# Kernel optimization log

Measured on AMD Instinct MI355X. Metric: run time of the kernel, lower is better.

## Reference

```python
import jax, jax.numpy as jnp
import numpy as np

EMBED_DIM = 2048
NUM_HEADS = 16
LATENT_DIM = 512
HEAD_DIM = EMBED_DIM // NUM_HEADS


def setup_inputs() -> dict:
    key = jax.random.key(0)
    ks = jax.random.split(key, 9)
    s = 0.02
    x = jax.random.normal(ks[0], (2, 2048, EMBED_DIM), dtype=jnp.float32)
    # torch Linear weights stored as [out, in]
    q_w = jax.random.normal(ks[1], (EMBED_DIM, EMBED_DIM), jnp.float32) * s
    q_b = jax.random.normal(ks[2], (EMBED_DIM,), jnp.float32) * s
    kvd_w = jax.random.normal(ks[3], (LATENT_DIM, EMBED_DIM), jnp.float32) * s
    kvd_b = jax.random.normal(ks[4], (LATENT_DIM,), jnp.float32) * s
    kvu_w = jax.random.normal(ks[5], (EMBED_DIM * 2, LATENT_DIM), jnp.float32) * s
    kvu_b = jax.random.normal(ks[6], (EMBED_DIM * 2,), jnp.float32) * s
    out_w = jax.random.normal(ks[7], (EMBED_DIM, EMBED_DIM), jnp.float32) * s
    out_b = jax.random.normal(ks[8], (EMBED_DIM,), jnp.float32) * s
    return {"x": x, "q_w": q_w, "q_b": q_b, "kvd_w": kvd_w, "kvd_b": kvd_b,
            "kvu_w": kvu_w, "kvu_b": kvu_b, "out_w": out_w, "out_b": out_b}


def reference(x, q_w, q_b, kvd_w, kvd_b, kvu_w, kvu_b, out_w, out_b):
    b, s, _ = x.shape
    q = x @ q_w.T + q_b                      # [b,s,E]
    latent = x @ kvd_w.T + kvd_b             # [b,s,L]
    kv = latent @ kvu_w.T + kvu_b            # [b,s,2E]
    k, v = kv[..., :EMBED_DIM], kv[..., EMBED_DIM:]
    def heads(t):
        return t.reshape(b, s, NUM_HEADS, HEAD_DIM).transpose(0, 2, 1, 3)  # [b,h,s,d]
    qh, kh, vh = heads(q), heads(k), heads(v)
    scores = jnp.einsum('bhqd,bhkd->bhqk', qh, kh) / jnp.sqrt(jnp.float32(HEAD_DIM))
    attn = jax.nn.softmax(scores, axis=-1)
    out = jnp.einsum('bhqk,bhkd->bhqd', attn, vh)
    out = out.transpose(0, 2, 1, 3).reshape(b, s, EMBED_DIM)
    return out @ out_w.T + out_b
```

## Files before the change

### kernel.cpp

```cpp
#include <hip/hip_runtime.h>

typedef unsigned short u16;
typedef __attribute__((ext_vector_type(8))) __bf16 bf16x8;
typedef __attribute__((ext_vector_type(8))) unsigned short u16x8;
typedef __attribute__((ext_vector_type(4))) float f32x4;
typedef __attribute__((ext_vector_type(16))) float f32x16;

#define BK 32
#define TILE_ELEMS (128 * BK)
#define QSCALE 0.12753706518066536f

#if __has_builtin(__builtin_amdgcn_exp2f)
#define EXP2(x) __builtin_amdgcn_exp2f(x)
#else
#define EXP2(x) exp2f(x)
#endif

__device__ __forceinline__ u16 f32_to_bf16(float f) {
  __bf16 h = (__bf16)f;
  return __builtin_bit_cast(u16, h);
}

__device__ __forceinline__ void gll16(const u16* g, u16* l) {
  __builtin_amdgcn_global_load_lds(
      (const __attribute__((address_space(1))) void*)g,
      (__attribute__((address_space(3))) void*)l, 16, 0, 0);
}

__global__ __launch_bounds__(256) void cvt_all(
    const float* __restrict__ x, const float* __restrict__ qw,
    const float* __restrict__ kvdw, const float* __restrict__ kvuw,
    const float* __restrict__ outw, u16* __restrict__ X, u16* __restrict__ W1,
    u16* __restrict__ W2, u16* __restrict__ W3, u16* __restrict__ W4) {
  int blk = blockIdx.x;
  const float* src;
  u16* dst;
  int base;
  if (blk < 8192)       { src = x;    dst = X;  base = blk; }
  else if (blk < 12288) { src = qw;   dst = W1; base = blk - 8192; }
  else if (blk < 13312) { src = kvdw; dst = W2; base = blk - 12288; }
  else if (blk < 15360) { src = kvuw; dst = W3; base = blk - 13312; }
  else                  { src = outw; dst = W4; base = blk - 15360; }
  int i = base * 1024 + threadIdx.x * 4;
  float4 v = *(const float4*)(src + i);
  ushort4 o;
  o.x = f32_to_bf16(v.x);
  o.y = f32_to_bf16(v.y);
  o.z = f32_to_bf16(v.z);
  o.w = f32_to_bf16(v.w);
  *(ushort4*)(dst + i) = o;
}

__device__ __forceinline__ void gemm_core(const u16* __restrict__ A_tile,
                                          const u16* __restrict__ B_tile, int K,
                                          u16* As, u16* Bs, f32x4 acc[4][4]) {
  const int tid = threadIdx.x;
  const int w = tid >> 6, lane = tid & 63;
  const int wm = (w >> 1) << 6, wn = (w & 1) << 6;
  const int quad = lane >> 4, l15 = lane & 15;

  const u16* Ap = A_tile + (tid >> 2) * K + (tid & 3) * 8;
  const u16* Bp = B_tile + (tid >> 2) * K + (tid & 3) * 8;
  u16* Asw = As + w * 512;
  u16* Bsw = Bs + w * 512;

  gll16(Ap, Asw);
  gll16(Ap + 64 * K, Asw + 2048);
  gll16(Bp, Bsw);
  gll16(Bp + 64 * K, Bsw + 2048);

  int p = 0;
  for (int k0 = 0; k0 < K; k0 += BK) {
    const int kn = k0 + BK;
    __syncthreads();
    if (kn < K) {
      const int off = (p ^ 1) * TILE_ELEMS;
      gll16(Ap + kn, Asw + off);
      gll16(Ap + 64 * K + kn, Asw + off + 2048);
      gll16(Bp + kn, Bsw + off);
      gll16(Bp + 64 * K + kn, Bsw + off + 2048);
    }
    const u16* Asr = As + p * TILE_ELEMS;
    const u16* Bsr = Bs + p * TILE_ELEMS;
    bf16x8 af[4], bf[4];
#pragma unroll
    for (int i = 0; i < 4; i++)
      af[i] = *(const bf16x8*)(Asr + (wm + i * 16 + l15) * BK + quad * 8);
#pragma unroll
    for (int j = 0; j < 4; j++)
      bf[j] = *(const bf16x8*)(Bsr + (wn + j * 16 + l15) * BK + quad * 8);
#pragma unroll
    for (int i = 0; i < 4; i++)
#pragma unroll
      for (int j = 0; j < 4; j++)
        acc[i][j] =
            __builtin_amdgcn_mfma_f32_16x16x32_bf16(af[i], bf[j], acc[i][j], 0, 0, 0);
    p ^= 1;
  }
}

__global__ __launch_bounds__(256) void gemm_qlat(const u16* __restrict__ X,
                                                 const u16* __restrict__ QW,
                                                 const u16* __restrict__ KVDW,
                                                 const float* __restrict__ q_b,
                                                 const float* __restrict__ kvd_b,
                                                 u16* __restrict__ Qb,
                                                 u16* __restrict__ Lat) {
  __shared__ __align__(16) u16 As[2 * TILE_ELEMS];
  __shared__ __align__(16) u16 Bs[2 * TILE_ELEMS];
  const int bn = blockIdx.x, bm = blockIdx.y;
  const bool isq = bn < 16;
  const u16* B_tile = isq ? QW + (size_t)bn * 128 * 2048
                          : KVDW + (size_t)(bn - 16) * 128 * 2048;
  f32x4 acc[4][4];
  const f32x4 z = {0.f, 0.f, 0.f, 0.f};
#pragma unroll
  for (int i = 0; i < 4; i++)
#pragma unroll
    for (int j = 0; j < 4; j++) acc[i][j] = z;
  gemm_core(X + (size_t)bm * 128 * 2048, B_tile, 2048, As, Bs, acc);

  const float* bias = isq ? q_b : kvd_b;
  u16* C = isq ? Qb : Lat;
  const int N = isq ? 2048 : 512;
  const float scale = isq ? QSCALE : 1.0f;
  const int colbase = (isq ? bn : bn - 16) * 128;

  const int tid = threadIdx.x;
  const int w = tid >> 6, lane = tid & 63;
  const int wm = (w >> 1) << 6, wn = (w & 1) << 6;
  const int quad = lane >> 4, l15 = lane & 15;
  const int row0 = bm * 128 + wm + quad * 4;
  const int col0 = colbase + wn + l15;
#pragma unroll
  for (int i = 0; i < 4; i++)
#pragma unroll
    for (int j = 0; j < 4; j++) {
      int col = col0 + j * 16;
      float bv = bias[col];
#pragma unroll
      for (int r = 0; r < 4; r++) {
        int row = row0 + i * 16 + r;
        C[(size_t)row * N + col] = f32_to_bf16((acc[i][j][r] + bv) * scale);
      }
    }
}

__global__ __launch_bounds__(256) void gemm_f32out(const u16* __restrict__ A,
                                                   const u16* __restrict__ B,
                                                   const float* __restrict__ bias,
                                                   float* __restrict__ C, int K, int N) {
  __shared__ __align__(16) u16 As[2 * TILE_ELEMS];
  __shared__ __align__(16) u16 Bs[2 * TILE_ELEMS];
  f32x4 acc[4][4];
  const f32x4 z = {0.f, 0.f, 0.f, 0.f};
#pragma unroll
  for (int i = 0; i < 4; i++)
#pragma unroll
    for (int j = 0; j < 4; j++) acc[i][j] = z;
  gemm_core(A + (size_t)blockIdx.y * 128 * K, B + (size_t)blockIdx.x * 128 * K, K,
            As, Bs, acc);

  const int tid = threadIdx.x;
  const int w = tid >> 6, lane = tid & 63;
  const int wm = (w >> 1) << 6, wn = (w & 1) << 6;
  const int quad = lane >> 4, l15 = lane & 15;
  const int row0 = blockIdx.y * 128 + wm + quad * 4;
  const int col0 = blockIdx.x * 128 + wn + l15;
#pragma unroll
  for (int i = 0; i < 4; i++)
#pragma unroll
    for (int j = 0; j < 4; j++) {
      int col = col0 + j * 16;
      float bv = bias[col];
#pragma unroll
      for (int r = 0; r < 4; r++) {
        int row = row0 + i * 16 + r;
        C[(size_t)row * N + col] = acc[i][j][r] + bv;
      }
    }
}

__global__ __launch_bounds__(256) void gemm_kv(const u16* __restrict__ A,
                                               const u16* __restrict__ B,
                                               const float* __restrict__ bias,
                                               u16* __restrict__ Khat,
                                               u16* __restrict__ Vt, int K) {
  __shared__ __align__(16) u16 As[2 * TILE_ELEMS];
  __shared__ __align__(16) u16 Bs[2 * TILE_ELEMS];
  f32x4 acc[4][4];
  const f32x4 z = {0.f, 0.f, 0.f, 0.f};
#pragma unroll
  for (int i = 0; i < 4; i++)
#pragma unroll
    for (int j = 0; j < 4; j++) acc[i][j] = z;
  gemm_core(A + (size_t)blockIdx.y * 128 * K, B + (size_t)blockIdx.x * 128 * K, K,
            As, Bs, acc);

  const int tid = threadIdx.x;
  const int w = tid >> 6, lane = tid & 63;
  const int wm = (w >> 1) << 6, wn = (w & 1) << 6;
  const int quad = lane >> 4, l15 = lane & 15;
  const int row0 = blockIdx.y * 128 + wm + quad * 4;
  const int col0 = blockIdx.x * 128 + wn + l15;
#pragma unroll
  for (int i = 0; i < 4; i++)
#pragma unroll
    for (int j = 0; j < 4; j++) {
      int n = col0 + j * 16;
      float bv = bias[n];
#pragma unroll
      for (int r = 0; r < 4; r++) {
        int row = row0 + i * 16 + r;
        int bb = row >> 11, s = row & 2047;
        u16 val = f32_to_bf16(acc[i][j][r] + bv);
        if (n < 2048) {
          int h = n >> 7, d = n & 127;
          Khat[((size_t)(bb * 16 + h) * 2048 + s) * 128 + d] = val;
        } else {
          int h = (n - 2048) >> 7, d = n & 127;
          Vt[((size_t)(bb * 16 + h) * 128 + d) * 2048 + s] = val;
        }
      }
    }
}

__global__ __launch_bounds__(256) void attn_kernel(const u16* __restrict__ Q,
                                                   const u16* __restrict__ Khat,
                                                   const u16* __restrict__ Vt,
                                                   u16* __restrict__ O) {
  __shared__ __align__(16) u16 Ks[2][32 * 136];
  __shared__ __align__(16) u16 Vs[2][128 * 40];

  const int tid = threadIdx.x;
  const int w = tid >> 6, lane = tid & 63;
  const int l31 = lane & 31, half = lane >> 5;
  const int qt = blockIdx.x & 15;
  const int h = (blockIdx.x >> 4) & 15;
  const int b = blockIdx.x >> 8;
  const int bh = b * 16 + h;

  bf16x8 qf[8];
  {
    const u16* qrow = Q + (size_t)(b * 2048 + qt * 128 + w * 32 + l31) * 2048 +
                      h * 128 + half * 8;
#pragma unroll
    for (int kc = 0; kc < 8; kc++) qf[kc] = *(const bf16x8*)(qrow + kc * 16);
  }

  f32x16 oacc[4];
#pragma unroll
  for (int nt = 0; nt < 4; nt++)
#pragma unroll
    for (int r = 0; r < 16; r++) oacc[nt][r] = 0.f;
  float ls0 = 0.f, ls1 = 0.f, ls2 = 0.f, ls3 = 0.f;

  const u16* Kg = Khat + (size_t)bh * 2048 * 128;
  const u16* Vg = Vt + (size_t)bh * 128 * 2048;

  const int kkr = tid >> 4, kc0 = tid & 15;
  const int vd = tid >> 2, vc0 = tid & 3;
  const int vlo = (vc0 >> 1) * 16 + (vc0 & 1) * 4;
  const int vhi = vlo + 8;

  u16x8 kv[2], vv[2];
#pragma unroll
  for (int it = 0; it < 2; it++) {
    kv[it] = *(const u16x8*)(Kg + (size_t)(kkr + it * 16) * 128 + kc0 * 8);
    vv[it] = *(const u16x8*)(Vg + (size_t)(vd + it * 64) * 2048 + vc0 * 8);
  }
#pragma unroll
  for (int it = 0; it < 2; it++) {
    *(u16x8*)(Ks[0] + (kkr + it * 16) * 136 + kc0 * 8) = kv[it];
    const unsigned long long* vp = (const unsigned long long*)&vv[it];
    *(unsigned long long*)(Vs[0] + (vd + it * 64) * 40 + vlo) = vp[0];
    *(unsigned long long*)(Vs[0] + (vd + it * 64) * 40 + vhi) = vp[1];
  }

  int p = 0;
  for (int key0 = 0; key0 < 2048; key0 += 32) {
    const int kn = (key0 + 32 < 2048) ? (key0 + 32) : 0;
#pragma unroll
    for (int it = 0; it < 2; it++) {
      kv[it] = *(const u16x8*)(Kg + (size_t)(kn + kkr + it * 16) * 128 + kc0 * 8);
      vv[it] = *(const u16x8*)(Vg + (size_t)(vd + it * 64) * 2048 + kn + vc0 * 8);
    }
    __syncthreads();

    f32x16 sacc;
#pragma unroll
    for (int r = 0; r < 16; r++) sacc[r] = 0.f;
#pragma unroll
    for (int kc = 0; kc < 8; kc++) {
      bf16x8 kf = *(const bf16x8*)(Ks[p] + l31 * 136 + kc * 16 + half * 8);
      sacc = __builtin_amdgcn_mfma_f32_32x32x16_bf16(kf, qf[kc], sacc, 0, 0, 0);
    }

    float e[16];
#pragma unroll
    for (int r = 0; r < 16; r++) e[r] = EXP2(sacc[r]);
    ls0 += e[0] + e[4] + e[8] + e[12];
    ls1 += e[1] + e[5] + e[9] + e[13];
    ls2 += e[2] + e[6] + e[10] + e[14];
    ls3 += e[3] + e[7] + e[11] + e[15];
    bf16x8 pa0, pa1;
#pragma unroll
    for (int i = 0; i < 8; i++) {
      pa0[i] = (__bf16)e[i];
      pa1[i] = (__bf16)e[8 + i];
    }

#pragma unroll
    for (int nt = 0; nt < 4; nt++) {
      bf16x8 vf0 = *(const bf16x8*)(Vs[p] + (nt * 32 + l31) * 40 + half * 8);
      bf16x8 vf1 = *(const bf16x8*)(Vs[p] + (nt * 32 + l31) * 40 + 16 + half * 8);
      oacc[nt] = __builtin_amdgcn_mfma_f32_32x32x16_bf16(pa0, vf0, oacc[nt], 0, 0, 0);
      oacc[nt] = __builtin_amdgcn_mfma_f32_32x32x16_bf16(pa1, vf1, oacc[nt], 0, 0, 0);
    }

    const int pn = p ^ 1;
#pragma unroll
    for (int it = 0; it < 2; it++) {
      *(u16x8*)(Ks[pn] + (kkr + it * 16) * 136 + kc0 * 8) = kv[it];
      const unsigned long long* vp = (const unsigned long long*)&vv[it];
      *(unsigned long long*)(Vs[pn] + (vd + it * 64) * 40 + vlo) = vp[0];
      *(unsigned long long*)(Vs[pn] + (vd + it * 64) * 40 + vhi) = vp[1];
    }
    p = pn;
  }

  float lsum = (ls0 + ls1) + (ls2 + ls3);
  lsum += __shfl_xor(lsum, 32);
  float inv = 1.0f / lsum;
  float wr[16];
#pragma unroll
  for (int r = 0; r < 16; r++) {
    int ridx = (r & 3) + 8 * (r >> 2) + 4 * half;
    wr[r] = __shfl(inv, ridx);
  }

#pragma unroll
  for (int nt = 0; nt < 4; nt++)
#pragma unroll
    for (int r = 0; r < 16; r++) {
      int ridx = (r & 3) + 8 * (r >> 2) + 4 * half;
      int row = b * 2048 + qt * 128 + w * 32 + ridx;
      int col = h * 128 + nt * 32 + l31;
      O[(size_t)row * 2048 + col] = f32_to_bf16(oacc[nt][r] * wr[r]);
    }
}

extern "C" void kernel_launch(void* const* d_in, const int* in_sizes, int n_in,
                              void* d_out, int out_size, void* d_ws, size_t ws_size,
                              hipStream_t stream) {
  (void)in_sizes; (void)n_in; (void)out_size; (void)ws_size;
  const float* x     = (const float*)d_in[0];
  const float* q_w   = (const float*)d_in[1];
  const float* q_b   = (const float*)d_in[2];
  const float* kvd_w = (const float*)d_in[3];
  const float* kvd_b = (const float*)d_in[4];
  const float* kvu_w = (const float*)d_in[5];
  const float* kvu_b = (const float*)d_in[6];
  const float* out_w = (const float*)d_in[7];
  const float* out_b = (const float*)d_in[8];
  float* out = (float*)d_out;

  char* p = (char*)d_ws;
  u16* X    = (u16*)(p + 0);
  u16* W1   = (u16*)(p + (size_t)16 * 1024 * 1024);
  u16* W2   = (u16*)(p + (size_t)24 * 1024 * 1024);
  u16* W3   = (u16*)(p + (size_t)26 * 1024 * 1024);
  u16* W4   = (u16*)(p + (size_t)30 * 1024 * 1024);
  u16* Qb   = (u16*)(p + (size_t)38 * 1024 * 1024);
  u16* Lat  = (u16*)(p + (size_t)54 * 1024 * 1024);
  u16* Khat = (u16*)(p + (size_t)58 * 1024 * 1024);
  u16* Vt   = (u16*)(p + (size_t)74 * 1024 * 1024);
  u16* AO   = (u16*)(p + (size_t)90 * 1024 * 1024);

  cvt_all<<<dim3(19456), dim3(256), 0, stream>>>(x, q_w, kvd_w, kvu_w, out_w,
                                                 X, W1, W2, W3, W4);
  gemm_qlat<<<dim3(20, 32), dim3(256), 0, stream>>>(X, W1, W2, q_b, kvd_b, Qb, Lat);
  gemm_kv<<<dim3(32, 32), dim3(256), 0, stream>>>(Lat, W3, kvu_b, Khat, Vt, 512);
  attn_kernel<<<dim3(512), dim3(256), 0, stream>>>(Qb, Khat, Vt, AO);
  gemm_f32out<<<dim3(16, 32), dim3(256), 0, stream>>>(AO, W4, out_b, out, 2048, 2048);
}
```

Baseline: 369.4 us.

## Split attention over the key dimension into two halves with a combine pass

Adds an attention path that splits the 2048 keys into two halves of 1024. This doubles the block count to 1024 and halves each block's serial loop. Each half writes unnormalised fp32 partial outputs and row sums to workspace, and a separate combine kernel adds them, normalises, and writes the bf16 attention output. The aim is better occupancy and latency hiding on the many CUs, at the cost of extra global traffic for the fp32 partials and one more launch. The path runs only when the workspace is at least 171 MB; otherwise the original attention kernel is used.

```diff
diff --git a/kernel.cpp b/kernel.cpp
--- a/kernel.cpp
+++ b/kernel.cpp
@@ -350,10 +350,164 @@
     }
 }
 
+__global__ __launch_bounds__(256) void attn_split(const u16* __restrict__ Q,
+                                                  const u16* __restrict__ Khat,
+                                                  const u16* __restrict__ Vt,
+                                                  float* __restrict__ Op,
+                                                  float* __restrict__ Ls) {
+  __shared__ __align__(16) u16 Ks[2][32 * 136];
+  __shared__ __align__(16) u16 Vs[2][128 * 40];
+
+  const int tid = threadIdx.x;
+  const int w = tid >> 6, lane = tid & 63;
+  const int l31 = lane & 31, half = lane >> 5;
+  const int qt = blockIdx.x & 15;
+  const int h = (blockIdx.x >> 4) & 15;
+  const int b = (blockIdx.x >> 8) & 1;
+  const int kh = blockIdx.x >> 9;
+  const int bh = b * 16 + h;
+  const int klo = kh * 1024, khi = klo + 1024;
+
+  bf16x8 qf[8];
+  {
+    const u16* qrow = Q + (size_t)(b * 2048 + qt * 128 + w * 32 + l31) * 2048 +
+                      h * 128 + half * 8;
+#pragma unroll
+    for (int kc = 0; kc < 8; kc++) qf[kc] = *(const bf16x8*)(qrow + kc * 16);
+  }
+
+  f32x16 oacc[4];
+#pragma unroll
+  for (int nt = 0; nt < 4; nt++)
+#pragma unroll
+    for (int r = 0; r < 16; r++) oacc[nt][r] = 0.f;
+  float ls0 = 0.f, ls1 = 0.f, ls2 = 0.f, ls3 = 0.f;
+
+  const u16* Kg = Khat + (size_t)bh * 2048 * 128;
+  const u16* Vg = Vt + (size_t)bh * 128 * 2048;
+
+  const int kkr = tid >> 4, kc0 = tid & 15;
+  const int vd = tid >> 2, vc0 = tid & 3;
+  const int vlo = (vc0 >> 1) * 16 + (vc0 & 1) * 4;
+  const int vhi = vlo + 8;
+
+  u16x8 kv[2], vv[2];
+#pragma unroll
+  for (int it = 0; it < 2; it++) {
+    kv[it] = *(const u16x8*)(Kg + (size_t)(klo + kkr + it * 16) * 128 + kc0 * 8);
+    vv[it] = *(const u16x8*)(Vg + (size_t)(vd + it * 64) * 2048 + klo + vc0 * 8);
+  }
+#pragma unroll
+  for (int it = 0; it < 2; it++) {
+    *(u16x8*)(Ks[0] + (kkr + it * 16) * 136 + kc0 * 8) = kv[it];
+    const unsigned long long* vp = (const unsigned long long*)&vv[it];
+    *(unsigned long long*)(Vs[0] + (vd + it * 64) * 40 + vlo) = vp[0];
+    *(unsigned long long*)(Vs[0] + (vd + it * 64) * 40 + vhi) = vp[1];
+  }
+
+  int p = 0;
+  for (int key0 = klo; key0 < khi; key0 += 32) {
+    const int kn = (key0 + 32 < khi) ? (key0 + 32) : klo;
+#pragma unroll
+    for (int it = 0; it < 2; it++) {
+      kv[it] = *(const u16x8*)(Kg + (size_t)(kn + kkr + it * 16) * 128 + kc0 * 8);
+      vv[it] = *(const u16x8*)(Vg + (size_t)(vd + it * 64) * 2048 + kn + vc0 * 8);
+    }
+    __syncthreads();
+
+    f32x16 sacc;
+#pragma unroll
+    for (int r = 0; r < 16; r++) sacc[r] = 0.f;
+#pragma unroll
+    for (int kc = 0; kc < 8; kc++) {
+      bf16x8 kf = *(const bf16x8*)(Ks[p] + l31 * 136 + kc * 16 + half * 8);
+      sacc = __builtin_amdgcn_mfma_f32_32x32x16_bf16(kf, qf[kc], sacc, 0, 0, 0);
+    }
+
+    float e[16];
+#pragma unroll
+    for (int r = 0; r < 16; r++) e[r] = EXP2(sacc[r]);
+    ls0 += e[0] + e[4] + e[8] + e[12];
+    ls1 += e[1] + e[5] + e[9] + e[13];
+    ls2 += e[2] + e[6] + e[10] + e[14];
+    ls3 += e[3] + e[7] + e[11] + e[15];
+    bf16x8 pa0, pa1;
+#pragma unroll
+    for (int i = 0; i < 8; i++) {
+      pa0[i] = (__bf16)e[i];
+      pa1[i] = (__bf16)e[8 + i];
+    }
+
+#pragma unroll
+    for (int nt = 0; nt < 4; nt++) {
+      bf16x8 vf0 = *(const bf16x8*)(Vs[p] + (nt * 32 + l31) * 40 + half * 8);
+      bf16x8 vf1 = *(const bf16x8*)(Vs[p] + (nt * 32 + l31) * 40 + 16 + half * 8);
+      oacc[nt] = __builtin_amdgcn_mfma_f32_32x32x16_bf16(pa0, vf0, oacc[nt], 0, 0, 0);
+      oacc[nt] = __builtin_amdgcn_mfma_f32_32x32x16_bf16(pa1, vf1, oacc[nt], 0, 0, 0);
+    }
+
+    const int pn = p ^ 1;
+#pragma unroll
+    for (int it = 0; it < 2; it++) {
+      *(u16x8*)(Ks[pn] + (kkr + it * 16) * 136 + kc0 * 8) = kv[it];
+      const unsigned long long* vp = (const unsigned long long*)&vv[it];
+      *(unsigned long long*)(Vs[pn] + (vd + it * 64) * 40 + vlo) = vp[0];
+      *(unsigned long long*)(Vs[pn] + (vd + it * 64) * 40 + vhi) = vp[1];
+    }
+    p = pn;
+  }
+
+  float lsum = (ls0 + ls1) + (ls2 + ls3);
+  lsum += __shfl_xor(lsum, 32);
+  if (lane < 32) {
+    Ls[(size_t)(kh * 32 + bh) * 2048 + qt * 128 + w * 32 + l31] = lsum;
+  }
+
+  float* Of = Op + (size_t)kh * 4096 * 2048;
+#pragma unroll
+  for (int nt = 0; nt < 4; nt++)
+#pragma unroll
+    for (int r = 0; r < 16; r++) {
+      int ridx = (r & 3) + 8 * (r >> 2) + 4 * half;
+      int row = b * 2048 + qt * 128 + w * 32 + ridx;
+      int col = h * 128 + nt * 32 + l31;
+      Of[(size_t)row * 2048 + col] = oacc[nt][r];
+    }
+}
+
+__global__ __launch_bounds__(256) void attn_combine(const float* __restrict__ Op,
+                                                    const float* __restrict__ Ls,
+                                                    u16* __restrict__ AO) {
+  const int row = blockIdx.x;
+  const int col0 = threadIdx.x * 8;
+  const int b = row >> 11, s = row & 2047;
+  const int h = col0 >> 7;
+  const int bh = b * 16 + h;
+  const float l0 = Ls[(size_t)bh * 2048 + s];
+  const float l1 = Ls[(size_t)(32 + bh) * 2048 + s];
+  const float inv = 1.0f / (l0 + l1);
+  const size_t base = (size_t)row * 2048 + col0;
+  const float4 a0 = *(const float4*)(Op + base);
+  const float4 a1 = *(const float4*)(Op + base + 4);
+  const float4 b0 = *(const float4*)(Op + (size_t)4096 * 2048 + base);
+  const float4 b1 = *(const float4*)(Op + (size_t)4096 * 2048 + base + 4);
+  ushort4 o0, o1;
+  o0.x = f32_to_bf16((a0.x + b0.x) * inv);
+  o0.y = f32_to_bf16((a0.y + b0.y) * inv);
+  o0.z = f32_to_bf16((a0.z + b0.z) * inv);
+  o0.w = f32_to_bf16((a0.w + b0.w) * inv);
+  o1.x = f32_to_bf16((a1.x + b1.x) * inv);
+  o1.y = f32_to_bf16((a1.y + b1.y) * inv);
+  o1.z = f32_to_bf16((a1.z + b1.z) * inv);
+  o1.w = f32_to_bf16((a1.w + b1.w) * inv);
+  *(ushort4*)(AO + base) = o0;
+  *(ushort4*)(AO + base + 4) = o1;
+}
+
 extern "C" void kernel_launch(void* const* d_in, const int* in_sizes, int n_in,
                               void* d_out, int out_size, void* d_ws, size_t ws_size,
                               hipStream_t stream) {
-  (void)in_sizes; (void)n_in; (void)out_size; (void)ws_size;
+  (void)in_sizes; (void)n_in; (void)out_size;
   const float* x     = (const float*)d_in[0];
   const float* q_w   = (const float*)d_in[1];
   const float* q_b   = (const float*)d_in[2];
@@ -376,11 +530,20 @@
   u16* Khat = (u16*)(p + (size_t)58 * 1024 * 1024);
   u16* Vt   = (u16*)(p + (size_t)74 * 1024 * 1024);
   u16* AO   = (u16*)(p + (size_t)90 * 1024 * 1024);
+  float* Op = (float*)(p + (size_t)106 * 1024 * 1024);
+  float* Ls = (float*)(p + (size_t)170 * 1024 * 1024);
+
+  const bool split = ws_size >= (size_t)171 * 1024 * 1024;
 
   cvt_all<<<dim3(19456), dim3(256), 0, stream>>>(x, q_w, kvd_w, kvu_w, out_w,
                                                  X, W1, W2, W3, W4);
   gemm_qlat<<<dim3(20, 32), dim3(256), 0, stream>>>(X, W1, W2, q_b, kvd_b, Qb, Lat);
   gemm_kv<<<dim3(32, 32), dim3(256), 0, stream>>>(Lat, W3, kvu_b, Khat, Vt, 512);
-  attn_kernel<<<dim3(512), dim3(256), 0, stream>>>(Qb, Khat, Vt, AO);
+  if (split) {
+    attn_split<<<dim3(1024), dim3(256), 0, stream>>>(Qb, Khat, Vt, Op, Ls);
+    attn_combine<<<dim3(4096), dim3(256), 0, stream>>>(Op, Ls, AO);
+  } else {
+    attn_kernel<<<dim3(512), dim3(256), 0, stream>>>(Qb, Khat, Vt, AO);
+  }
   gemm_f32out<<<dim3(16, 32), dim3(256), 0, stream>>>(AO, W4, out_b, out, 2048, 2048);
 }
```

Result: slower. 400.8 us (+8.5%).
